# Kernel tuning notes

Hardware: AMD Instinct MI355X
Metric: run time of the kernel (lower is better)

Reference implementation:

```python
import jax, jax.numpy as jnp
import numpy as np

EPS = 1e-8
TAU = 0.2  # gumbel temperature


def lorentz_linear(x, W, log_scale):
    # y = W x; project back onto hyperboloid (k=1): time from sigmoid, rescale space
    y = x @ W.T
    time = jax.nn.sigmoid(y[..., :1]) * jnp.exp(log_scale) + 1.1
    narrow = y[..., 1:]
    s = (time * time - 1.0) / jnp.clip(jnp.sum(narrow * narrow, axis=-1, keepdims=True), EPS, None)
    return jnp.concatenate([time, narrow * jnp.sqrt(s)], axis=-1)


def logmap0(x):
    # Lorentz (k=1) log map at origin o=(1,0,...,0): (0, arccosh(x0) * xs/||xs||)
    x0 = x[..., :1]
    xs = x[..., 1:]
    nrm = jnp.clip(jnp.linalg.norm(xs, axis=-1, keepdims=True), EPS, None)
    d = jnp.arccosh(jnp.clip(x0, 1.0 + 1e-6, None))
    return jnp.concatenate([jnp.zeros_like(x0), d * xs / nrm], axis=-1)


def lorentz_dist(a, b):
    # dist = arccosh(-<a,b>_L), <a,b>_L = -a0*b0 + sum_i ai*bi
    inner = a[..., 0] * b[..., 0] - jnp.sum(a[..., 1:] * b[..., 1:], axis=-1)
    return jnp.arccosh(jnp.clip(inner, 1.0 + 1e-6, None))


def scatter_softmax(score, seg, num_segments):
    m = jax.ops.segment_max(score, seg, num_segments=num_segments)
    m = jnp.where(jnp.isfinite(m), m, 0.0)  # empty segments
    e = jnp.exp(score - m[seg])
    s = jax.ops.segment_sum(e, seg, num_segments=num_segments)
    return e / jnp.clip(s[seg], EPS, None)


def setup_inputs() -> dict:
    key = jax.random.key(0)
    ks = jax.random.split(key, 8)
    N, E, D, A = 50000, 800000, 128, 128
    # nodes on hyperboloid: time = sqrt(1 + ||space||^2)
    xs = jax.random.normal(ks[0], (N, D - 1), dtype=jnp.float32)
    x0 = jnp.sqrt(1.0 + jnp.sum(xs * xs, axis=-1, keepdims=True))
    x = jnp.concatenate([x0, xs], axis=-1)
    src = jax.random.randint(ks[1], (E,), 0, N)
    dst = jax.random.randint(ks[2], (E,), 0, N)
    edge_value = jax.random.uniform(ks[3], (E,), dtype=jnp.float32)
    stdv = 1.0 / np.sqrt(D)
    Wq = jax.random.uniform(ks[4], (D, D), minval=-stdv, maxval=stdv, dtype=jnp.float32).at[:, 0].set(0.0)
    Wk = jax.random.uniform(ks[5], (D, D), minval=-stdv, maxval=stdv, dtype=jnp.float32).at[:, 0].set(0.0)
    Wa = jax.random.normal(ks[6], (A, D), dtype=jnp.float32) * np.sqrt(2.0 / (A + D))
    log_scale = jnp.asarray(np.log(10.0), dtype=jnp.float32)
    return {"x": x, "src": src, "dst": dst, "edge_value": edge_value,
            "Wq": Wq, "Wk": Wk, "Wa": Wa,
            "log_scale_q": log_scale, "log_scale_k": log_scale}


def reference(x, src, dst, edge_value, Wq, Wk, Wa, log_scale_q, log_scale_k):
    N = x.shape[0]
    # assignment logits in tangent space -> softmax
    ass = jax.nn.softmax(logmap0(x) @ Wa.T, axis=-1)  # [N, A]
    q = lorentz_linear(x, Wq, log_scale_q)            # [N, D]
    k = lorentz_linear(x, Wk, log_scale_k)
    # per-edge negative Lorentz distance
    score = -lorentz_dist(q[src], k[dst])             # [E]
    # scatter softmax over outgoing edges of each src node
    score = scatter_softmax(score, src, N)
    # sparse attention matmul: out[i] = sum_{e: src=i} score_e * ass[dst_e]
    ass = jax.ops.segment_sum(score[:, None] * ass[dst], src, num_segments=N)  # [N, A]
    # gumbel softmax on log(ass + 1e-6)
    logits = jnp.log(ass + 1e-6)
    u = jax.random.uniform(jax.random.key(42), logits.shape, minval=1e-10, maxval=1.0)
    g = -jnp.log(-jnp.log(u))
    return jax.nn.softmax((logits + g) / TAU, axis=-1)
```

## Files before the change

### kernel.cpp

```cpp
#include <hip/hip_runtime.h>
#include <hip/hip_bf16.h>
#include <hip/hip_fp16.h>
#include <math.h>


#define D128 128
#define XP 136

typedef _Float16 f16x2 __attribute__((ext_vector_type(2)));
typedef _Float16 f16x8 __attribute__((ext_vector_type(8)));
typedef float f32x4 __attribute__((ext_vector_type(4)));

union U4 { uint4 u; f16x2 f2[4]; __half2 hh[4]; };

__device__ __forceinline__ void threefry2x32(unsigned x0, unsigned x1,
                                             unsigned& o0, unsigned& o1) {
  const unsigned k0 = 0u, k1 = 42u;
  const unsigned k2 = 0x1BD11BDAu ^ k0 ^ k1;
  x0 += k0; x1 += k1;
#define TF_ROT(r) { x0 += x1; x1 = (x1 << (r)) | (x1 >> (32 - (r))); x1 ^= x0; }
  TF_ROT(13) TF_ROT(15) TF_ROT(26) TF_ROT(6)
  x0 += k1; x1 += k2 + 1u;
  TF_ROT(17) TF_ROT(29) TF_ROT(16) TF_ROT(24)
  x0 += k2; x1 += k0 + 2u;
  TF_ROT(13) TF_ROT(15) TF_ROT(26) TF_ROT(6)
  x0 += k0; x1 += k1 + 3u;
  TF_ROT(17) TF_ROT(29) TF_ROT(16) TF_ROT(24)
  x0 += k1; x1 += k2 + 4u;
  TF_ROT(13) TF_ROT(15) TF_ROT(26) TF_ROT(6)
  x0 += k2; x1 += k0 + 5u;
#undef TF_ROT
  o0 = x0; o1 = x1;
}

__global__ __launch_bounds__(256) void cvt_count_kernel(
    const float* __restrict__ Wq, const float* __restrict__ Wk,
    const float* __restrict__ Wa, __half* __restrict__ wqh,
    __half* __restrict__ wkh, __half* __restrict__ wah,
    const int* __restrict__ src, int* __restrict__ counts, int E) {
  int b = blockIdx.x;
  if (b < 24) {
    int i = b * 256 + threadIdx.x;
    int w = i >> 11, r = i & 2047;
    if (w >= 3) return;
    size_t off = (size_t)r * 8;
    const float* s = (w == 0) ? Wq : (w == 1) ? Wk : Wa;
    __half* d = (w == 0) ? wqh : (w == 1) ? wkh : wah;
    float4 a = *reinterpret_cast<const float4*>(s + off);
    float4 c = *reinterpret_cast<const float4*>(s + off + 4);
    union { __half2 h2[4]; uint4 u; } pk;
    pk.h2[0] = __floats2half2_rn(a.x, a.y);
    pk.h2[1] = __floats2half2_rn(a.z, a.w);
    pk.h2[2] = __floats2half2_rn(c.x, c.y);
    pk.h2[3] = __floats2half2_rn(c.z, c.w);
    *reinterpret_cast<uint4*>(d + off) = pk.u;
  } else {
    int e = (b - 24) * 256 + threadIdx.x;
    if (e < E) atomicAdd(&counts[src[e]], 1);
  }
}

__global__ __launch_bounds__(256) void gemm3_kernel(
    const float* __restrict__ X, const __half* __restrict__ wqh_g,
    const __half* __restrict__ wkh_g, const __half* __restrict__ wah_g,
    const float* __restrict__ lsq, const float* __restrict__ lsk,
    __half* __restrict__ qout, __half* __restrict__ kout,
    __half* __restrict__ aout, int N) {
  __shared__ __align__(16) _Float16 xs[64 * XP];
  __shared__ __align__(16) _Float16 wh[128 * XP];

  const int t = threadIdx.x;
  const int row0 = blockIdx.x * 64;

#pragma unroll
  for (int i = 0; i < 8; ++i) {
    int f = t + 256 * i, r = f >> 5, c4 = f & 31;
    float4 v = make_float4(0.f, 0.f, 0.f, 0.f);
    if (row0 + r < N)
      v = *reinterpret_cast<const float4*>(X + (size_t)(row0 + r) * D128 + c4 * 4);
    union { _Float16 h[4]; uint2 u; } p;
    p.h[0] = (_Float16)v.x; p.h[1] = (_Float16)v.y;
    p.h[2] = (_Float16)v.z; p.h[3] = (_Float16)v.w;
    *reinterpret_cast<uint2*>(&xs[r * XP + c4 * 4]) = p.u;
  }

  const int w = t >> 6, lane = t & 63;
  const int lc = lane & 15;
  const int arow = 16 * w + lc;
  const int koff = (lane >> 4) * 8;

  for (int p = 0; p < 3; ++p) {
    __syncthreads();
    const __half* Wg = (p == 0) ? wqh_g : (p == 1) ? wkh_g : wah_g;
#pragma unroll
    for (int i = 0; i < 8; ++i) {
      int f = t + 256 * i, wr = f >> 4, c8 = f & 15;
      *reinterpret_cast<uint4*>(&wh[wr * XP + c8 * 8]) =
          *reinterpret_cast<const uint4*>(Wg + (size_t)wr * D128 + c8 * 8);
    }

    if (p == 2) {
#pragma unroll
      for (int rr = 0; rr < 2; ++rr) {
        int r = (t >> 3) + 32 * rr, tr = t & 7;
        U4 c0, c1;
        c0.u = *reinterpret_cast<uint4*>(&xs[r * XP + tr * 16]);
        c1.u = *reinterpret_cast<uint4*>(&xs[r * XP + tr * 16 + 8]);
        float v[16];
        float ss = 0.f;
#pragma unroll
        for (int j = 0; j < 4; ++j) {
          float2 f = __half22float2(c0.hh[j]);
          v[2 * j] = f.x; v[2 * j + 1] = f.y; ss += f.x * f.x + f.y * f.y;
        }
#pragma unroll
        for (int j = 0; j < 4; ++j) {
          float2 f = __half22float2(c1.hh[j]);
          v[8 + 2 * j] = f.x; v[9 + 2 * j] = f.y; ss += f.x * f.x + f.y * f.y;
        }
        if (tr == 0) ss -= v[0] * v[0];
#pragma unroll
        for (int msk = 1; msk < 8; msk <<= 1) ss += __shfl_xor(ss, msk);
        float x0v = __shfl(v[0], (t & 63) & ~7);
        float dd = acoshf(fmaxf(x0v, 1.f + 1e-6f));
        float sc = dd / fmaxf(sqrtf(ss), 1e-8f);
#pragma unroll
        for (int j = 0; j < 16; ++j) v[j] *= sc;
        if (tr == 0) v[0] = 0.f;
        union { __half2 h2[4]; uint4 u; } pk;
#pragma unroll
        for (int j = 0; j < 4; ++j) pk.h2[j] = __floats2half2_rn(v[2 * j], v[2 * j + 1]);
        *reinterpret_cast<uint4*>(&xs[r * XP + tr * 16]) = pk.u;
#pragma unroll
        for (int j = 0; j < 4; ++j) pk.h2[j] = __floats2half2_rn(v[8 + 2 * j], v[9 + 2 * j]);
        *reinterpret_cast<uint4*>(&xs[r * XP + tr * 16 + 8]) = pk.u;
      }
    }
    __syncthreads();

    f32x4 acc[8];
#pragma unroll
    for (int i = 0; i < 8; ++i) acc[i] = (f32x4){0.f, 0.f, 0.f, 0.f};
#pragma unroll
    for (int kk = 0; kk < 4; ++kk) {
      f16x8 a = *reinterpret_cast<f16x8*>(&xs[arow * XP + kk * 32 + koff]);
#pragma unroll
      for (int tt = 0; tt < 8; ++tt) {
        f16x8 b = *reinterpret_cast<f16x8*>(&wh[(tt * 16 + lc) * XP + kk * 32 + koff]);
        acc[tt] = __builtin_amdgcn_mfma_f32_16x16x32_f16(a, b, acc[tt], 0, 0, 0);
      }
    }

    if (p < 2) {
      float scale = expf(p ? lsk[0] : lsq[0]);
      __half* outp = p ? kout : qout;
      float sgn = p ? 1.f : -1.f;
#pragma unroll
      for (int j = 0; j < 4; ++j) {
        int gr = row0 + 16 * w + ((lane >> 4) << 2) + j;
        float ss = 0.f;
#pragma unroll
        for (int tt = 0; tt < 8; ++tt) {
          float v = acc[tt][j];
          if (tt == 0 && lc == 0) v = 0.f;
          ss += v * v;
        }
#pragma unroll
        for (int msk = 1; msk < 16; msk <<= 1) ss += __shfl_xor(ss, msk);
        float y0 = __shfl(acc[0][j], lane & ~15);
        float tm = scale / (1.f + expf(-y0)) + 1.1f;
        float qs = sqrtf((tm * tm - 1.f) / fmaxf(ss, 1e-8f)) * sgn;
        if (gr < N) {
#pragma unroll
          for (int tt = 0; tt < 8; ++tt) {
            float val = acc[tt][j] * qs;
            if (tt == 0 && lc == 0) val = tm;
            outp[(size_t)gr * D128 + tt * 16 + lc] = __float2half(val);
          }
        }
      }
    } else {
#pragma unroll
      for (int j = 0; j < 4; ++j) {
        int gr = row0 + 16 * w + ((lane >> 4) << 2) + j;
        float mx = acc[0][j];
#pragma unroll
        for (int tt = 1; tt < 8; ++tt) mx = fmaxf(mx, acc[tt][j]);
#pragma unroll
        for (int msk = 1; msk < 16; msk <<= 1) mx = fmaxf(mx, __shfl_xor(mx, msk));
        float e[8], sm = 0.f;
#pragma unroll
        for (int tt = 0; tt < 8; ++tt) { e[tt] = expf(acc[tt][j] - mx); sm += e[tt]; }
#pragma unroll
        for (int msk = 1; msk < 16; msk <<= 1) sm += __shfl_xor(sm, msk);
        float inv = 1.f / sm;
        if (gr < N) {
#pragma unroll
          for (int tt = 0; tt < 8; ++tt)
            aout[(size_t)gr * D128 + tt * 16 + lc] = __float2half(e[tt] * inv);
        }
      }
    }
  }
}

__global__ __launch_bounds__(256) void scan1_kernel(const int* __restrict__ counts,
                                                    int* __restrict__ incl,
                                                    int* __restrict__ partials, int N) {
  int i = blockIdx.x * 256 + threadIdx.x;
  int c = (i < N) ? counts[i] : 0;
  int lane = threadIdx.x & 63, w = threadIdx.x >> 6;
  int v = c;
#pragma unroll
  for (int d = 1; d < 64; d <<= 1) {
    int tv = __shfl_up(v, d);
    if (lane >= d) v += tv;
  }
  __shared__ int wsum[4];
  if (lane == 63) wsum[w] = v;
  __syncthreads();
  int add = 0;
  for (int j = 0; j < w; ++j) add += wsum[j];
  v += add;
  if (i < N) incl[i] = v;
  if (threadIdx.x == 255) partials[blockIdx.x] = v;
}

__global__ __launch_bounds__(256) void scan2_kernel(int* __restrict__ partials, int nparts) {
  int t = threadIdx.x;
  int p = (t < nparts) ? partials[t] : 0;
  int lane = t & 63, w = t >> 6;
  int v = p;
#pragma unroll
  for (int d = 1; d < 64; d <<= 1) {
    int tv = __shfl_up(v, d);
    if (lane >= d) v += tv;
  }
  __shared__ int wsum[4];
  if (lane == 63) wsum[w] = v;
  __syncthreads();
  int add = 0;
  for (int j = 0; j < w; ++j) add += wsum[j];
  v += add;
  if (t < nparts) partials[t] = v - p;
}

__global__ __launch_bounds__(256) void scan3_kernel(const int* __restrict__ counts,
                                                    int* __restrict__ incl_to_start,
                                                    int* __restrict__ cursor,
                                                    const int* __restrict__ partials, int N) {
  int i = blockIdx.x * 256 + threadIdx.x;
  if (i < N) {
    int s = incl_to_start[i] - counts[i] + partials[blockIdx.x];
    incl_to_start[i] = s;
    cursor[i] = s;
  }
}

__global__ __launch_bounds__(256) void csr_fill_kernel(
    const int* __restrict__ src, const int* __restrict__ dst,
    int* __restrict__ cursor, int* __restrict__ dst_s, int E) {
  int e = blockIdx.x * 256 + threadIdx.x;
  if (e < E) {
    int pos = atomicAdd(&cursor[src[e]], 1);
    dst_s[pos] = dst[e];
  }
}

__global__ __launch_bounds__(256) void node_fused_kernel(
    const __half* __restrict__ qh, const __half* __restrict__ kh,
    const __half* __restrict__ ass, const int* __restrict__ start,
    const int* __restrict__ counts, const int* __restrict__ dst_s,
    float* __restrict__ out, int N) {
  int g = threadIdx.x >> 4;
  int lq = threadIdx.x & 15;
  int n = blockIdx.x * 16 + g;
  if (n >= N) return;
  int st = start[n], deg = counts[n];
  int c8 = lq * 8;

  U4 qv;
  qv.u = *reinterpret_cast<const uint4*>(qh + (size_t)n * D128 + c8);

  float lsum = 0.f;
  float acc[8];
#pragma unroll
  for (int j = 0; j < 8; ++j) acc[j] = 0.f;

  if (deg > 0) {
    int d0 = dst_s[st];
    int d1 = (deg > 1) ? dst_s[st + 1] : d0;
    U4 kv0, av0, kv1, av1;
    kv0.u = *reinterpret_cast<const uint4*>(kh + (size_t)d0 * D128 + c8);
    av0.u = *reinterpret_cast<const uint4*>(ass + (size_t)d0 * D128 + c8);
    kv1.u = *reinterpret_cast<const uint4*>(kh + (size_t)d1 * D128 + c8);
    av1.u = *reinterpret_cast<const uint4*>(ass + (size_t)d1 * D128 + c8);

    for (int i = 0; i < deg; ++i) {
      int p2 = st + i + 2;
      int d2 = dst_s[(p2 < st + deg) ? p2 : st];
      U4 kv2, av2;
      kv2.u = *reinterpret_cast<const uint4*>(kh + (size_t)d2 * D128 + c8);
      av2.u = *reinterpret_cast<const uint4*>(ass + (size_t)d2 * D128 + c8);

      float pa = __builtin_amdgcn_fdot2(qv.f2[0], kv0.f2[0],
                 __builtin_amdgcn_fdot2(qv.f2[1], kv0.f2[1], 0.f, false), false);
      float pb = __builtin_amdgcn_fdot2(qv.f2[2], kv0.f2[2],
                 __builtin_amdgcn_fdot2(qv.f2[3], kv0.f2[3], 0.f, false), false);
      float part = pa + pb;
#pragma unroll
      for (int msk = 1; msk < 16; msk <<= 1) part += __shfl_xor(part, msk);

      float x = fmaxf(part, 1.f + 1e-6f);
      float tt = x + sqrtf(__builtin_fmaf(x, x, -1.f));
      float w = __builtin_amdgcn_rcpf(tt);

      lsum += w;
      float2 v0 = __half22float2(av0.hh[0]);
      float2 v1 = __half22float2(av0.hh[1]);
      float2 v2 = __half22float2(av0.hh[2]);
      float2 v3 = __half22float2(av0.hh[3]);
      acc[0] += w * v0.x;  acc[1] += w * v0.y;
      acc[2] += w * v1.x;  acc[3] += w * v1.y;
      acc[4] += w * v2.x;  acc[5] += w * v2.y;
      acc[6] += w * v3.x;  acc[7] += w * v3.y;

      kv0 = kv1; av0 = av1;
      kv1 = kv2; av1 = av2;
    }
  }

  float inv = (deg > 0) ? 1.f / fmaxf(lsum, 1e-8f) : 0.f;

  float vg[8];
#pragma unroll
  for (int j = 0; j < 8; ++j) {
    unsigned o0, o1;
    threefry2x32(0u, (unsigned)(n * D128 + c8 + j), o0, o1);
    unsigned bits = o0 ^ o1;
    float f = __uint_as_float((bits >> 9) | 0x3f800000u) - 1.0f;
    float u = fmaxf(1e-10f, f * (1.0f - 1e-10f) + 1e-10f);
    float gmb = -logf(-logf(u));
    vg[j] = (logf(acc[j] * inv + 1e-6f) + gmb) / 0.2f;
  }
  float mm = vg[0];
#pragma unroll
  for (int j = 1; j < 8; ++j) mm = fmaxf(mm, vg[j]);
#pragma unroll
  for (int msk = 1; msk < 16; msk <<= 1) mm = fmaxf(mm, __shfl_xor(mm, msk));
  float sm = 0.f;
#pragma unroll
  for (int j = 0; j < 8; ++j) { vg[j] = expf(vg[j] - mm); sm += vg[j]; }
#pragma unroll
  for (int msk = 1; msk < 16; msk <<= 1) sm += __shfl_xor(sm, msk);
  float invs = 1.f / sm;
  *reinterpret_cast<float4*>(out + (size_t)n * D128 + c8) =
      make_float4(vg[0] * invs, vg[1] * invs, vg[2] * invs, vg[3] * invs);
  *reinterpret_cast<float4*>(out + (size_t)n * D128 + c8 + 4) =
      make_float4(vg[4] * invs, vg[5] * invs, vg[6] * invs, vg[7] * invs);
}

extern "C" void kernel_launch(void* const* d_in, const int* in_sizes, int n_in,
                              void* d_out, int out_size, void* d_ws, size_t ws_size,
                              hipStream_t stream) {
  const float* x   = (const float*)d_in[0];
  const int*   src = (const int*)d_in[1];
  const int*   dst = (const int*)d_in[2];
  const float* Wq  = (const float*)d_in[4];
  const float* Wk  = (const float*)d_in[5];
  const float* Wa  = (const float*)d_in[6];
  const float* lsq = (const float*)d_in[7];
  const float* lsk = (const float*)d_in[8];
  const int N = in_sizes[0] / D128;
  const int E = in_sizes[1];
  float* out = (float*)d_out;

  __half* qh   = (__half*)d_ws;
  __half* kh   = qh + (size_t)N * D128;
  __half* ah   = kh + (size_t)N * D128;
  __half* wqh  = ah + (size_t)N * D128;
  __half* wkh  = wqh + 16384;
  __half* wah  = wkh + 16384;
  int* counts  = (int*)(wah + 16384);
  int* startv  = counts + N;
  int* cursor  = startv + N;
  int* partials= cursor + N;
  int* dst_s   = partials + 256;

  hipMemsetAsync(counts, 0, (size_t)N * sizeof(int), stream);

  const int eb = (E + 255) / 256;
  cvt_count_kernel<<<24 + eb, 256, 0, stream>>>(Wq, Wk, Wa, wqh, wkh, wah,
                                                src, counts, E);

  const int gemm_blocks = (N + 63) / 64;
  gemm3_kernel<<<gemm_blocks, 256, 0, stream>>>(x, wqh, wkh, wah, lsq, lsk,
                                                qh, kh, ah, N);

  const int nb = (N + 255) / 256;
  scan1_kernel<<<nb, 256, 0, stream>>>(counts, startv, partials, N);
  scan2_kernel<<<1, 256, 0, stream>>>(partials, nb);
  scan3_kernel<<<nb, 256, 0, stream>>>(counts, startv, cursor, partials, N);
  csr_fill_kernel<<<eb, 256, 0, stream>>>(src, dst, cursor, dst_s, E);

  node_fused_kernel<<<(N + 15) / 16, 256, 0, stream>>>(qh, kh, ah, startv,
                                                       counts, dst_s, out, N);
}
```

Before: 207.7 us.

## Sort nodes by degree for balanced aggregation and retile the projection GEMM

Builds a degree histogram and counting-sort permutation so the per-node fused aggregation kernel processes nodes of similar degree together, reducing divergence within waves. The GEMM kernel now handles 128 rows per block and streams each weight matrix in two 64-row halves, reusing each weight tile across two row tiles. The gather prefetch depth in the node kernel drops from two edges ahead to one. This adds atomics in the scan kernels and one extra indirection per node, and scatters output writes across the output.

```diff
diff --git a/kernel.cpp b/kernel.cpp
--- a/kernel.cpp
+++ b/kernel.cpp
@@ -66,14 +66,14 @@
     const float* __restrict__ lsq, const float* __restrict__ lsk,
     __half* __restrict__ qout, __half* __restrict__ kout,
     __half* __restrict__ aout, int N) {
-  __shared__ __align__(16) _Float16 xs[64 * XP];
-  __shared__ __align__(16) _Float16 wh[128 * XP];
+  __shared__ __align__(16) _Float16 xs[128 * XP];
+  __shared__ __align__(16) _Float16 wh[64 * XP];
 
   const int t = threadIdx.x;
-  const int row0 = blockIdx.x * 64;
-
-#pragma unroll
-  for (int i = 0; i < 8; ++i) {
+  const int row0 = blockIdx.x * 128;
+
+#pragma unroll
+  for (int i = 0; i < 16; ++i) {
     int f = t + 256 * i, r = f >> 5, c4 = f & 31;
     float4 v = make_float4(0.f, 0.f, 0.f, 0.f);
     if (row0 + r < N)
@@ -86,22 +86,15 @@
 
   const int w = t >> 6, lane = t & 63;
   const int lc = lane & 15;
-  const int arow = 16 * w + lc;
   const int koff = (lane >> 4) * 8;
 
-  for (int p = 0; p < 3; ++p) {
-    __syncthreads();
-    const __half* Wg = (p == 0) ? wqh_g : (p == 1) ? wkh_g : wah_g;
-#pragma unroll
-    for (int i = 0; i < 8; ++i) {
-      int f = t + 256 * i, wr = f >> 4, c8 = f & 15;
-      *reinterpret_cast<uint4*>(&wh[wr * XP + c8 * 8]) =
-          *reinterpret_cast<const uint4*>(Wg + (size_t)wr * D128 + c8 * 8);
-    }
-
-    if (p == 2) {
-#pragma unroll
-      for (int rr = 0; rr < 2; ++rr) {
+  for (int m = 0; m < 3; ++m) {
+    const __half* Wg = (m == 0) ? wqh_g : (m == 1) ? wkh_g : wah_g;
+
+    if (m == 2) {
+      __syncthreads();
+#pragma unroll
+      for (int rr = 0; rr < 4; ++rr) {
         int r = (t >> 3) + 32 * rr, tr = t & 7;
         U4 c0, c1;
         c0.u = *reinterpret_cast<uint4*>(&xs[r * XP + tr * 16]);
@@ -136,68 +129,91 @@
         *reinterpret_cast<uint4*>(&xs[r * XP + tr * 16 + 8]) = pk.u;
       }
     }
-    __syncthreads();
-
-    f32x4 acc[8];
-#pragma unroll
-    for (int i = 0; i < 8; ++i) acc[i] = (f32x4){0.f, 0.f, 0.f, 0.f};
-#pragma unroll
-    for (int kk = 0; kk < 4; ++kk) {
-      f16x8 a = *reinterpret_cast<f16x8*>(&xs[arow * XP + kk * 32 + koff]);
-#pragma unroll
-      for (int tt = 0; tt < 8; ++tt) {
-        f16x8 b = *reinterpret_cast<f16x8*>(&wh[(tt * 16 + lc) * XP + kk * 32 + koff]);
-        acc[tt] = __builtin_amdgcn_mfma_f32_16x16x32_f16(a, b, acc[tt], 0, 0, 0);
-      }
-    }
-
-    if (p < 2) {
-      float scale = expf(p ? lsk[0] : lsq[0]);
-      __half* outp = p ? kout : qout;
-      float sgn = p ? 1.f : -1.f;
-#pragma unroll
-      for (int j = 0; j < 4; ++j) {
-        int gr = row0 + 16 * w + ((lane >> 4) << 2) + j;
-        float ss = 0.f;
-#pragma unroll
-        for (int tt = 0; tt < 8; ++tt) {
-          float v = acc[tt][j];
-          if (tt == 0 && lc == 0) v = 0.f;
-          ss += v * v;
-        }
-#pragma unroll
-        for (int msk = 1; msk < 16; msk <<= 1) ss += __shfl_xor(ss, msk);
-        float y0 = __shfl(acc[0][j], lane & ~15);
-        float tm = scale / (1.f + expf(-y0)) + 1.1f;
-        float qs = sqrtf((tm * tm - 1.f) / fmaxf(ss, 1e-8f)) * sgn;
-        if (gr < N) {
-#pragma unroll
-          for (int tt = 0; tt < 8; ++tt) {
-            float val = acc[tt][j] * qs;
-            if (tt == 0 && lc == 0) val = tm;
-            outp[(size_t)gr * D128 + tt * 16 + lc] = __float2half(val);
+
+    f32x4 acc[2][8];
+#pragma unroll
+    for (int rt = 0; rt < 2; ++rt)
+#pragma unroll
+      for (int i = 0; i < 8; ++i) acc[rt][i] = (f32x4){0.f, 0.f, 0.f, 0.f};
+
+    for (int h = 0; h < 2; ++h) {
+      __syncthreads();
+#pragma unroll
+      for (int i = 0; i < 4; ++i) {
+        int f = t + 256 * i, wr = f >> 4, c8 = f & 15;
+        *reinterpret_cast<uint4*>(&wh[wr * XP + c8 * 8]) =
+            *reinterpret_cast<const uint4*>(Wg + (size_t)(64 * h + wr) * D128 + c8 * 8);
+      }
+      __syncthreads();
+
+#pragma unroll
+      for (int rt = 0; rt < 2; ++rt) {
+#pragma unroll
+        for (int kk = 0; kk < 4; ++kk) {
+          f16x8 a = *reinterpret_cast<f16x8*>(&xs[(64 * rt + 16 * w + lc) * XP + kk * 32 + koff]);
+#pragma unroll
+          for (int tt = 0; tt < 4; ++tt) {
+            f16x8 b = *reinterpret_cast<f16x8*>(&wh[(tt * 16 + lc) * XP + kk * 32 + koff]);
+            acc[rt][h * 4 + tt] =
+                __builtin_amdgcn_mfma_f32_16x16x32_f16(a, b, acc[rt][h * 4 + tt], 0, 0, 0);
           }
         }
       }
+    }
+
+    if (m < 2) {
+      float scale = expf(m ? lsk[0] : lsq[0]);
+      __half* outp = m ? kout : qout;
+      float sgn = m ? 1.f : -1.f;
+#pragma unroll
+      for (int rt = 0; rt < 2; ++rt) {
+#pragma unroll
+        for (int j = 0; j < 4; ++j) {
+          int gr = row0 + 64 * rt + 16 * w + ((lane >> 4) << 2) + j;
+          float ss = 0.f;
+#pragma unroll
+          for (int ct = 0; ct < 8; ++ct) {
+            float v = acc[rt][ct][j];
+            if (ct == 0 && lc == 0) v = 0.f;
+            ss += v * v;
+          }
+#pragma unroll
+          for (int msk = 1; msk < 16; msk <<= 1) ss += __shfl_xor(ss, msk);
+          float y0 = __shfl(acc[rt][0][j], lane & ~15);
+          float tm = scale / (1.f + expf(-y0)) + 1.1f;
+          float qs = sqrtf((tm * tm - 1.f) / fmaxf(ss, 1e-8f)) * sgn;
+          if (gr < N) {
+#pragma unroll
+            for (int ct = 0; ct < 8; ++ct) {
+              float val = acc[rt][ct][j] * qs;
+              if (ct == 0 && lc == 0) val = tm;
+              outp[(size_t)gr * D128 + ct * 16 + lc] = __float2half(val);
+            }
+          }
+        }
+      }
     } else {
 #pragma unroll
-      for (int j = 0; j < 4; ++j) {
-        int gr = row0 + 16 * w + ((lane >> 4) << 2) + j;
-        float mx = acc[0][j];
-#pragma unroll
-        for (int tt = 1; tt < 8; ++tt) mx = fmaxf(mx, acc[tt][j]);
-#pragma unroll
-        for (int msk = 1; msk < 16; msk <<= 1) mx = fmaxf(mx, __shfl_xor(mx, msk));
-        float e[8], sm = 0.f;
-#pragma unroll
-        for (int tt = 0; tt < 8; ++tt) { e[tt] = expf(acc[tt][j] - mx); sm += e[tt]; }
-#pragma unroll
-        for (int msk = 1; msk < 16; msk <<= 1) sm += __shfl_xor(sm, msk);
-        float inv = 1.f / sm;
-        if (gr < N) {
-#pragma unroll
-          for (int tt = 0; tt < 8; ++tt)
-            aout[(size_t)gr * D128 + tt * 16 + lc] = __float2half(e[tt] * inv);
+      for (int rt = 0; rt < 2; ++rt) {
+#pragma unroll
+        for (int j = 0; j < 4; ++j) {
+          int gr = row0 + 64 * rt + 16 * w + ((lane >> 4) << 2) + j;
+          float mx = acc[rt][0][j];
+#pragma unroll
+          for (int ct = 1; ct < 8; ++ct) mx = fmaxf(mx, acc[rt][ct][j]);
+#pragma unroll
+          for (int msk = 1; msk < 16; msk <<= 1) mx = fmaxf(mx, __shfl_xor(mx, msk));
+          float e[8], sm = 0.f;
+#pragma unroll
+          for (int ct = 0; ct < 8; ++ct) { e[ct] = expf(acc[rt][ct][j] - mx); sm += e[ct]; }
+#pragma unroll
+          for (int msk = 1; msk < 16; msk <<= 1) sm += __shfl_xor(sm, msk);
+          float inv = 1.f / sm;
+          if (gr < N) {
+#pragma unroll
+            for (int ct = 0; ct < 8; ++ct)
+              aout[(size_t)gr * D128 + ct * 16 + lc] = __float2half(e[ct] * inv);
+          }
         }
       }
     }
@@ -206,9 +222,11 @@
 
 __global__ __launch_bounds__(256) void scan1_kernel(const int* __restrict__ counts,
                                                     int* __restrict__ incl,
-                                                    int* __restrict__ partials, int N) {
+                                                    int* __restrict__ partials,
+                                                    int* __restrict__ dhist, int N) {
   int i = blockIdx.x * 256 + threadIdx.x;
   int c = (i < N) ? counts[i] : 0;
+  if (i < N) atomicAdd(&dhist[c < 255 ? c : 255], 1);
   int lane = threadIdx.x & 63, w = threadIdx.x >> 6;
   int v = c;
 #pragma unroll
@@ -226,34 +244,57 @@
   if (threadIdx.x == 255) partials[blockIdx.x] = v;
 }
 
-__global__ __launch_bounds__(256) void scan2_kernel(int* __restrict__ partials, int nparts) {
+__global__ __launch_bounds__(256) void scan2_kernel(int* __restrict__ partials, int nparts,
+                                                    const int* __restrict__ dhist,
+                                                    int* __restrict__ dcursor) {
   int t = threadIdx.x;
+  int lane = t & 63, w = t >> 6;
+  __shared__ int wsum[4];
+
   int p = (t < nparts) ? partials[t] : 0;
-  int lane = t & 63, w = t >> 6;
   int v = p;
 #pragma unroll
   for (int d = 1; d < 64; d <<= 1) {
     int tv = __shfl_up(v, d);
     if (lane >= d) v += tv;
   }
-  __shared__ int wsum[4];
   if (lane == 63) wsum[w] = v;
   __syncthreads();
   int add = 0;
   for (int j = 0; j < w; ++j) add += wsum[j];
   v += add;
   if (t < nparts) partials[t] = v - p;
+  __syncthreads();
+
+  int hv = dhist[t];
+  int v2 = hv;
+#pragma unroll
+  for (int d = 1; d < 64; d <<= 1) {
+    int tv = __shfl_up(v2, d);
+    if (lane >= d) v2 += tv;
+  }
+  if (lane == 63) wsum[w] = v2;
+  __syncthreads();
+  int add2 = 0;
+  for (int j = 0; j < w; ++j) add2 += wsum[j];
+  v2 += add2;
+  dcursor[t] = v2 - hv;
 }
 
 __global__ __launch_bounds__(256) void scan3_kernel(const int* __restrict__ counts,
                                                     int* __restrict__ incl_to_start,
                                                     int* __restrict__ cursor,
-                                                    const int* __restrict__ partials, int N) {
+                                                    const int* __restrict__ partials,
+                                                    int* __restrict__ dcursor,
+                                                    int* __restrict__ perm, int N) {
   int i = blockIdx.x * 256 + threadIdx.x;
   if (i < N) {
-    int s = incl_to_start[i] - counts[i] + partials[blockIdx.x];
+    int c = counts[i];
+    int s = incl_to_start[i] - c + partials[blockIdx.x];
     incl_to_start[i] = s;
     cursor[i] = s;
+    int pos = atomicAdd(&dcursor[c < 255 ? c : 255], 1);
+    perm[pos] = i;
   }
 }
 
@@ -271,11 +312,12 @@
     const __half* __restrict__ qh, const __half* __restrict__ kh,
     const __half* __restrict__ ass, const int* __restrict__ start,
     const int* __restrict__ counts, const int* __restrict__ dst_s,
-    float* __restrict__ out, int N) {
+    const int* __restrict__ perm, float* __restrict__ out, int N) {
   int g = threadIdx.x >> 4;
   int lq = threadIdx.x & 15;
-  int n = blockIdx.x * 16 + g;
-  if (n >= N) return;
+  int idx = blockIdx.x * 16 + g;
+  if (idx >= N) return;
+  int n = perm[idx];
   int st = start[n], deg = counts[n];
   int c8 = lq * 8;
 
@@ -288,25 +330,23 @@
   for (int j = 0; j < 8; ++j) acc[j] = 0.f;
 
   if (deg > 0) {
-    int d0 = dst_s[st];
-    int d1 = (deg > 1) ? dst_s[st + 1] : d0;
-    U4 kv0, av0, kv1, av1;
-    kv0.u = *reinterpret_cast<const uint4*>(kh + (size_t)d0 * D128 + c8);
-    av0.u = *reinterpret_cast<const uint4*>(ass + (size_t)d0 * D128 + c8);
-    kv1.u = *reinterpret_cast<const uint4*>(kh + (size_t)d1 * D128 + c8);
-    av1.u = *reinterpret_cast<const uint4*>(ass + (size_t)d1 * D128 + c8);
+    int d_cur = dst_s[st];
+    int d_nxt = (deg > 1) ? dst_s[st + 1] : d_cur;
+    U4 kv, av;
+    kv.u = *reinterpret_cast<const uint4*>(kh + (size_t)d_cur * D128 + c8);
+    av.u = *reinterpret_cast<const uint4*>(ass + (size_t)d_cur * D128 + c8);
 
     for (int i = 0; i < deg; ++i) {
+      U4 kvn, avn;
+      kvn.u = *reinterpret_cast<const uint4*>(kh + (size_t)d_nxt * D128 + c8);
+      avn.u = *reinterpret_cast<const uint4*>(ass + (size_t)d_nxt * D128 + c8);
       int p2 = st + i + 2;
-      int d2 = dst_s[(p2 < st + deg) ? p2 : st];
-      U4 kv2, av2;
-      kv2.u = *reinterpret_cast<const uint4*>(kh + (size_t)d2 * D128 + c8);
-      av2.u = *reinterpret_cast<const uint4*>(ass + (size_t)d2 * D128 + c8);
-
-      float pa = __builtin_amdgcn_fdot2(qv.f2[0], kv0.f2[0],
-                 __builtin_amdgcn_fdot2(qv.f2[1], kv0.f2[1], 0.f, false), false);
-      float pb = __builtin_amdgcn_fdot2(qv.f2[2], kv0.f2[2],
-                 __builtin_amdgcn_fdot2(qv.f2[3], kv0.f2[3], 0.f, false), false);
+      int d_nn = dst_s[(p2 < st + deg) ? p2 : st];
+
+      float pa = __builtin_amdgcn_fdot2(qv.f2[0], kv.f2[0],
+                 __builtin_amdgcn_fdot2(qv.f2[1], kv.f2[1], 0.f, false), false);
+      float pb = __builtin_amdgcn_fdot2(qv.f2[2], kv.f2[2],
+                 __builtin_amdgcn_fdot2(qv.f2[3], kv.f2[3], 0.f, false), false);
       float part = pa + pb;
 #pragma unroll
       for (int msk = 1; msk < 16; msk <<= 1) part += __shfl_xor(part, msk);
@@ -316,17 +356,14 @@
       float w = __builtin_amdgcn_rcpf(tt);
 
       lsum += w;
-      float2 v0 = __half22float2(av0.hh[0]);
-      float2 v1 = __half22float2(av0.hh[1]);
-      float2 v2 = __half22float2(av0.hh[2]);
-      float2 v3 = __half22float2(av0.hh[3]);
-      acc[0] += w * v0.x;  acc[1] += w * v0.y;
-      acc[2] += w * v1.x;  acc[3] += w * v1.y;
-      acc[4] += w * v2.x;  acc[5] += w * v2.y;
-      acc[6] += w * v3.x;  acc[7] += w * v3.y;
-
-      kv0 = kv1; av0 = av1;
-      kv1 = kv2; av1 = av2;
+#pragma unroll
+      for (int j = 0; j < 4; ++j) {
+        acc[2 * j]     = fmaf(w, (float)av.f2[j][0], acc[2 * j]);
+        acc[2 * j + 1] = fmaf(w, (float)av.f2[j][1], acc[2 * j + 1]);
+      }
+
+      kv = kvn; av = avn;
+      d_nxt = d_nn;
     }
   }
 
@@ -382,27 +419,31 @@
   __half* wkh  = wqh + 16384;
   __half* wah  = wkh + 16384;
   int* counts  = (int*)(wah + 16384);
-  int* startv  = counts + N;
+  int* dhist   = counts + N;
+  int* startv  = dhist + 256;
   int* cursor  = startv + N;
   int* partials= cursor + N;
-  int* dst_s   = partials + 256;
-
-  hipMemsetAsync(counts, 0, (size_t)N * sizeof(int), stream);
+  int* dcursor = partials + 256;
+  int* perm    = dcursor + 256;
+  int* dst_s   = perm + N;
+
+  hipMemsetAsync(counts, 0, (size_t)(N + 256) * sizeof(int), stream);
 
   const int eb = (E + 255) / 256;
   cvt_count_kernel<<<24 + eb, 256, 0, stream>>>(Wq, Wk, Wa, wqh, wkh, wah,
                                                 src, counts, E);
 
-  const int gemm_blocks = (N + 63) / 64;
+  const int gemm_blocks = (N + 127) / 128;
   gemm3_kernel<<<gemm_blocks, 256, 0, stream>>>(x, wqh, wkh, wah, lsq, lsk,
                                                 qh, kh, ah, N);
 
   const int nb = (N + 255) / 256;
-  scan1_kernel<<<nb, 256, 0, stream>>>(counts, startv, partials, N);
-  scan2_kernel<<<1, 256, 0, stream>>>(partials, nb);
-  scan3_kernel<<<nb, 256, 0, stream>>>(counts, startv, cursor, partials, N);
+  scan1_kernel<<<nb, 256, 0, stream>>>(counts, startv, partials, dhist, N);
+  scan2_kernel<<<1, 256, 0, stream>>>(partials, nb, dhist, dcursor);
+  scan3_kernel<<<nb, 256, 0, stream>>>(counts, startv, cursor, partials,
+                                       dcursor, perm, N);
   csr_fill_kernel<<<eb, 256, 0, stream>>>(src, dst, cursor, dst_s, E);
 
   node_fused_kernel<<<(N + 15) / 16, 256, 0, stream>>>(qh, kh, ah, startv,
-                                                       counts, dst_s, out, N);
-}
+                                                       counts, dst_s, perm, out, N);
+}
```

After: 408.6 us. +96.7%, slower.
